# Kernel optimization log

Measured on AMD Instinct MI355X. Metric: run time of the kernel, lower is better.

The kernel has to match this reference:

```python
import math
import jax, jax.numpy as jnp
import numpy as np

B, T, N_FEAT, H = 16, 1024, 512, 8
D_K = N_FEAT // H  # 64


def setup_inputs() -> dict:
    key = jax.random.key(0)
    ks = jax.random.split(key, 16)
    s = 0.02
    return {
        "query": jax.random.normal(ks[0], (B, T, N_FEAT), jnp.float32),
        "key": jax.random.normal(ks[1], (B, T, N_FEAT), jnp.float32),
        "value": jax.random.normal(ks[2], (B, T, N_FEAT), jnp.float32),
        "pos_emb": jax.random.normal(ks[3], (1, T, N_FEAT), jnp.float32),
        "mask": jnp.zeros((B, 1, T), jnp.float32),  # additive bias, 0 = attend
        "Wq": jax.random.normal(ks[4], (N_FEAT, N_FEAT), jnp.float32) * s,
        "bq": jnp.zeros((N_FEAT,), jnp.float32),
        "Wk": jax.random.normal(ks[5], (N_FEAT, N_FEAT), jnp.float32) * s,
        "bk": jnp.zeros((N_FEAT,), jnp.float32),
        "Wv": jax.random.normal(ks[6], (N_FEAT, N_FEAT), jnp.float32) * s,
        "bv": jnp.zeros((N_FEAT,), jnp.float32),
        "Wo": jax.random.normal(ks[7], (N_FEAT, N_FEAT), jnp.float32) * s,
        "bo": jnp.zeros((N_FEAT,), jnp.float32),
        "Wpos": jax.random.normal(ks[8], (N_FEAT, N_FEAT), jnp.float32) * s,
        "pos_bias_u": jax.random.normal(ks[9], (H, D_K), jnp.float32) * 0.05,
        "pos_bias_v": jax.random.normal(ks[10], (H, D_K), jnp.float32) * 0.05,
    }


def reference(query, key, value, pos_emb, mask,
              Wq, bq, Wk, bk, Wv, bv, Wo, bo, Wpos,
              pos_bias_u, pos_bias_v):
    b, t, _ = query.shape
    h, d_k = pos_bias_u.shape
    # projections -> head-split
    q = (query @ Wq + bq).reshape(b, t, h, d_k)                 # (B,T,H,D)
    k = (key @ Wk + bk).reshape(b, -1, h, d_k).transpose(0, 2, 1, 3)    # (B,H,S,D)
    v = (value @ Wv + bv).reshape(b, -1, h, d_k).transpose(0, 2, 1, 3)  # (B,H,S,D)
    p = (pos_emb @ Wpos).reshape(pos_emb.shape[1], h, d_k).transpose(1, 0, 2)  # (H,S,D)
    # Transformer-XL content/position biased queries
    q_u = (q + pos_bias_u).transpose(0, 2, 1, 3)  # (B,H,T,D)
    q_v = (q + pos_bias_v).transpose(0, 2, 1, 3)  # (B,H,T,D)
    matrix_ac = jnp.einsum('bhtd,bhsd->bhts', q_u, k)
    matrix_bd = jnp.einsum('bhtd,hsd->bhts', q_v, p)
    scores = (matrix_ac + matrix_bd) / math.sqrt(d_k) + mask[:, None]  # (B,H,T,S)
    attn = jax.nn.softmax(scores, axis=-1)
    out = jnp.einsum('bhts,bhsd->bthd', attn, v).reshape(b, t, h * d_k)
    return out @ Wo + bo  # (B,T,n_feat)
```

## Files before the change

kernel.cpp:

```cpp
#include <hip/hip_runtime.h>

#define BB 16
#define TT 1024
#define HH 8
#define DD 64
#define NF 512

typedef __attribute__((ext_vector_type(4))) float f4;
typedef __attribute__((ext_vector_type(8))) short s8;
typedef __attribute__((ext_vector_type(2))) unsigned int u32x2;
typedef unsigned short u16;
typedef unsigned int u32;

#define LOG2E 1.4426950408889634f

__device__ __forceinline__ u16 f2bf(float x){
    unsigned int u = __builtin_bit_cast(unsigned int, x);
    u = (u + 0x7FFFu + ((u >> 16) & 1u)) >> 16;
    return (u16)u;
}
__device__ __forceinline__ float bf2f(u16 h){
    unsigned int u = ((unsigned int)h) << 16;
    return __builtin_bit_cast(float, u);
}
__device__ __forceinline__ u32 cvt_pk(float a, float b){
    u32 r; asm("v_cvt_pk_bf16_f32 %0, %1, %2" : "=v"(r) : "v"(a), "v"(b)); return r;
}
__device__ __forceinline__ float lo_bf(u32 p){ return __builtin_bit_cast(float, p << 16); }
__device__ __forceinline__ float hi_bf(u32 p){ return __builtin_bit_cast(float, p & 0xFFFF0000u); }

__global__ __launch_bounds__(256) void prep_w(const float* __restrict__ Wq,
    const float* __restrict__ Wk, const float* __restrict__ Wv,
    const float* __restrict__ Wpos, const float* __restrict__ Wo,
    u16* __restrict__ wtq, u16* __restrict__ wtk, u16* __restrict__ wtv,
    u16* __restrict__ wtp, u16* __restrict__ wohi, u16* __restrict__ wolo)
{
    __shared__ float tile[32][33];
    const int which = blockIdx.z;
    const float* W = which==0?Wq:which==1?Wk:which==2?Wv:which==3?Wpos:Wo;
    const int n0 = blockIdx.x*32, k0 = blockIdx.y*32;
    const int tc = threadIdx.x & 31, tr = threadIdx.x >> 5;
#pragma unroll
    for (int i=0;i<4;i++){ int r = tr + i*8; tile[r][tc] = W[(size_t)(k0+r)*NF + n0+tc]; }
    __syncthreads();
#pragma unroll
    for (int i=0;i<4;i++){
        int n = tr + i*8, k = tc;
        float val = tile[k][n];
        u16 hi = f2bf(val);
        size_t off = (size_t)(n0+n)*NF + k0+k;
        if (which==0) wtq[off]=hi; else if (which==1) wtk[off]=hi;
        else if (which==2) wtv[off]=hi; else if (which==3) wtp[off]=hi;
        else { wohi[off]=hi; wolo[off]=f2bf(val - bf2f(hi)); }
    }
}

template<int MODE>
__global__ __launch_bounds__(256) void gemm_bf16(const float* __restrict__ A,
                                                 const u16* __restrict__ Wt,
                                                 const float* __restrict__ bias,
                                                 const u16* __restrict__ padd,
                                                 u16* __restrict__ out)
{
    __shared__ __align__(16) u16 As[128*64];
    __shared__ __align__(16) u16 Bs[128*64];
    const int tid = threadIdx.x;
    const int row0 = blockIdx.x*128, col0 = blockIdx.y*128;
    const int wid = tid>>6, lane = tid&63, lm = lane&15, lg = lane>>4;
    const int wm = wid>>1, wn = wid&1;

    f4 acc[4][4];
#pragma unroll
    for (int i=0;i<4;i++)
#pragma unroll
        for (int j=0;j<4;j++) acc[i][j] = (f4){0.f,0.f,0.f,0.f};

    for (int k0=0;k0<NF;k0+=64){
        f4 areg[8]; s8 breg[4];
#pragma unroll
        for (int it=0; it<8; ++it){
            int idx = (it*256 + tid)*4;
            int m = idx>>6, k = idx&63;
            areg[it] = *(const f4*)(&A[(size_t)(row0+m)*NF + k0 + k]);
        }
#pragma unroll
        for (int it=0; it<4; ++it){
            int idx = (it*256 + tid)*8;
            int n = idx>>6, k = idx&63;
            breg[it] = *(const s8*)(&Wt[(size_t)(col0+n)*NF + k0 + k]);
        }
        __syncthreads();
#pragma unroll
        for (int it=0; it<8; ++it){
            int idx = (it*256+tid)*4;
            int m = idx>>6, k = idx&63;
            u32x2 pk;
            pk[0] = cvt_pk(areg[it][0], areg[it][1]);
            pk[1] = cvt_pk(areg[it][2], areg[it][3]);
            *(u32x2*)((char*)As + ((m*128 + k*2) ^ ((m&7)<<4))) = pk;
        }
#pragma unroll
        for (int it=0; it<4; ++it){
            int idx = (it*256+tid)*8;
            int n = idx>>6, k = idx&63;
            *(s8*)((char*)Bs + ((n*128 + k*2) ^ ((n&7)<<4))) = breg[it];
        }
        __syncthreads();
        s8 af[4][2], bf[4][2];
#pragma unroll
        for (int i=0;i<4;i++){
            int m = wm*64 + i*16 + lm;
#pragma unroll
            for (int c=0;c<2;c++)
                af[i][c] = *(const s8*)((char*)As + ((m*128 + c*64 + lg*16) ^ ((m&7)<<4)));
        }
#pragma unroll
        for (int j=0;j<4;j++){
            int n = wn*64 + j*16 + lm;
#pragma unroll
            for (int c=0;c<2;c++)
                bf[j][c] = *(const s8*)((char*)Bs + ((n*128 + c*64 + lg*16) ^ ((n&7)<<4)));
        }
#pragma unroll
        for (int i=0;i<4;i++)
#pragma unroll
            for (int j=0;j<4;j++)
#pragma unroll
                for (int c=0;c<2;c++)
                    acc[i][j] = __builtin_amdgcn_mfma_f32_16x16x32_bf16(af[i][c], bf[j][c], acc[i][j], 0,0,0);
    }

#pragma unroll
    for (int i=0;i<4;i++){
#pragma unroll
        for (int j=0;j<4;j++){
#pragma unroll
            for (int r=0;r<4;r++){
                const int m = row0 + wm*64 + i*16 + lg*4 + r;
                const int n = col0 + wn*64 + j*16 + lm;
                float val = acc[i][j][r];
                const int hh = n>>6, dd = n&63;
                if (MODE == 0){
                    out[(size_t)(hh*TT + m)*64 + dd] = f2bf(val);
                } else {
                    val += bias[n];
                    const int b_ = m>>10, t_ = m&1023;
                    if (MODE == 2) val += bf2f(padd[(size_t)(hh*TT + t_)*64 + dd]);
                    if (MODE == 3)
                        out[(((size_t)(b_*HH+hh))*DD + dd)*TT + t_] = f2bf(val);
                    else
                        out[((size_t)(b_*HH+hh)*TT + t_)*64 + dd] = f2bf(val);
                }
            }
        }
    }
}

__global__ __launch_bounds__(256) void gemm_final(const float* __restrict__ A,
    const u16* __restrict__ Bhg, const u16* __restrict__ Blg,
    const float* __restrict__ bias, float* __restrict__ out)
{
    __shared__ __align__(16) u16 Ah[128*64];
    __shared__ __align__(16) u16 Al[128*64];
    __shared__ __align__(16) u16 Bh[128*64];
    __shared__ __align__(16) u16 Bl[128*64];
    const int tid = threadIdx.x;
    const int row0 = blockIdx.x*128, col0 = blockIdx.y*128;
    const int wid = tid>>6, lane = tid&63, lm = lane&15, lg = lane>>4;
    const int wm = wid>>1, wn = wid&1;

    f4 acc[4][4];
#pragma unroll
    for (int i=0;i<4;i++)
#pragma unroll
        for (int j=0;j<4;j++) acc[i][j] = (f4){0.f,0.f,0.f,0.f};

    for (int k0=0;k0<NF;k0+=64){
        f4 areg[8]; s8 bhreg[4], blreg[4];
#pragma unroll
        for (int it=0; it<8; ++it){
            int idx = (it*256 + tid)*4;
            int m = idx>>6, k = idx&63;
            areg[it] = *(const f4*)(&A[(size_t)(row0+m)*NF + k0 + k]);
        }
#pragma unroll
        for (int it=0; it<4; ++it){
            int idx = (it*256 + tid)*8;
            int n = idx>>6, k = idx&63;
            bhreg[it] = *(const s8*)(&Bhg[(size_t)(col0+n)*NF + k0 + k]);
            blreg[it] = *(const s8*)(&Blg[(size_t)(col0+n)*NF + k0 + k]);
        }
        __syncthreads();
#pragma unroll
        for (int it=0; it<8; ++it){
            int idx = (it*256+tid)*4;
            int m = idx>>6, k = idx&63;
            u32 p0 = cvt_pk(areg[it][0], areg[it][1]);
            u32 p1 = cvt_pk(areg[it][2], areg[it][3]);
            u32 q0 = cvt_pk(areg[it][0]-lo_bf(p0), areg[it][1]-hi_bf(p0));
            u32 q1 = cvt_pk(areg[it][2]-lo_bf(p1), areg[it][3]-hi_bf(p1));
            int off = (m*128 + k*2) ^ ((m&7)<<4);
            *(u32x2*)((char*)Ah + off) = (u32x2){p0,p1};
            *(u32x2*)((char*)Al + off) = (u32x2){q0,q1};
        }
#pragma unroll
        for (int it=0; it<4; ++it){
            int idx = (it*256+tid)*8;
            int n = idx>>6, k = idx&63;
            int off = (n*128 + k*2) ^ ((n&7)<<4);
            *(s8*)((char*)Bh + off) = bhreg[it];
            *(s8*)((char*)Bl + off) = blreg[it];
        }
        __syncthreads();
#pragma unroll
        for (int c=0;c<2;c++){
            s8 ah[4], al[4], bh4[4], bl4[4];
#pragma unroll
            for (int i=0;i<4;i++){
                int m = wm*64 + i*16 + lm;
                int off = (m*128 + c*64 + lg*16) ^ ((m&7)<<4);
                ah[i] = *(const s8*)((char*)Ah + off);
                al[i] = *(const s8*)((char*)Al + off);
            }
#pragma unroll
            for (int j=0;j<4;j++){
                int n = wn*64 + j*16 + lm;
                int off = (n*128 + c*64 + lg*16) ^ ((n&7)<<4);
                bh4[j] = *(const s8*)((char*)Bh + off);
                bl4[j] = *(const s8*)((char*)Bl + off);
            }
#pragma unroll
            for (int i=0;i<4;i++)
#pragma unroll
                for (int j=0;j<4;j++){
                    acc[i][j] = __builtin_amdgcn_mfma_f32_16x16x32_bf16(al[i], bh4[j], acc[i][j], 0,0,0);
                    acc[i][j] = __builtin_amdgcn_mfma_f32_16x16x32_bf16(ah[i], bl4[j], acc[i][j], 0,0,0);
                    acc[i][j] = __builtin_amdgcn_mfma_f32_16x16x32_bf16(ah[i], bh4[j], acc[i][j], 0,0,0);
                }
        }
    }

#pragma unroll
    for (int i=0;i<4;i++)
#pragma unroll
        for (int j=0;j<4;j++)
#pragma unroll
            for (int r=0;r<4;r++){
                const int m = row0 + wm*64 + i*16 + lg*4 + r;
                const int n = col0 + wn*64 + j*16 + lm;
                out[(size_t)m*NF + n] = acc[i][j][r] + bias[n];
            }
}

__global__ __launch_bounds__(256) void sbias_kernel(const u16* __restrict__ kp,
                                                    const u16* __restrict__ p,
                                                    const float* __restrict__ pbu,
                                                    const float* __restrict__ pbv,
                                                    const float* __restrict__ mask,
                                                    float* __restrict__ sb)
{
    const int w    = blockIdx.x * 4 + (threadIdx.x >> 6);
    const int lane = threadIdx.x & 63;
    const int s = w & 1023;
    const int h = (w >> 10) & 7;
    const int b = w >> 13;
    const float u  = pbu[h * 64 + lane];
    const float wv = pbv[h * 64 + lane] - u;
    const float kv = bf2f(kp[((size_t)(b * HH + h) * TT + s) * 64 + lane]);
    const float pv = bf2f(p[(size_t)(h * TT + s) * 64 + lane]);
    float val = u * kv + wv * pv;
#pragma unroll
    for (int off = 32; off; off >>= 1) val += __shfl_xor(val, off);
    if (lane == 0)
        sb[(size_t)(b * HH + h) * TT + s] = (val * 0.125f + mask[b * TT + s]) * LOG2E;
}

#define ATTN_GLOAD(tile) do { \
  _Pragma("unroll") for (int it=0; it<2; ++it){ \
    int idx = (it*256+tid)*8; int row_ = idx>>6, col_ = idx&63; \
    kh[it] = *(const s8*)(kb + (size_t)((tile)*64+row_)*64 + col_); \
    vh[it] = *(const s8*)(vtb + (size_t)row_*TT + (tile)*64 + col_); } } while(0)

#define ATTN_SSTORE(buf) do { \
  _Pragma("unroll") for (int it=0; it<2; ++it){ \
    int idx = (it*256+tid)*8; int row_ = idx>>6, col_ = idx&63; \
    int off_ = (row_*128 + col_*2) ^ ((row_&7)<<4); \
    *(s8*)((char*)Ks[(buf)] + off_) = kh[it]; \
    *(s8*)((char*)Vt[(buf)] + off_) = vh[it]; } } while(0)

#define ATTN_QK(buf, scv) do { \
  _Pragma("unroll") for (int j=0;j<4;j++){ \
    int srow_ = j*16+lm; \
    s8 kf0 = *(const s8*)((char*)Ks[(buf)] + ((srow_*128 + lg*16) ^ ((srow_&7)<<4))); \
    s8 kf1 = *(const s8*)((char*)Ks[(buf)] + ((srow_*128 + 64 + lg*16) ^ ((srow_&7)<<4))); \
    scv[j] = __builtin_amdgcn_mfma_f32_16x16x32_bf16(kf0, qf[0], scv[j], 0,0,0); \
    scv[j] = __builtin_amdgcn_mfma_f32_16x16x32_bf16(kf1, qf[1], scv[j], 0,0,0); } } while(0)

__global__ __launch_bounds__(256,3) void attn4(const u16* __restrict__ q,
                                               const u16* __restrict__ kp,
                                               const u16* __restrict__ vt,
                                               const float* __restrict__ sb,
                                               float* __restrict__ ao)
{
    __shared__ __align__(16) u16 Ks[2][64*64];
    __shared__ __align__(16) u16 Vt[2][64*64];
    __shared__ __align__(16) u16 Ps[64*64];

    const int tid = threadIdx.x;
    const int wid = tid>>6, lane = tid&63, lm = lane&15, lg = lane>>4;
    const int bid = blockIdx.x;
    const int xcd = bid & 7, slot = bid >> 3;
    const int bh = xcd + 8*(slot >> 4);
    const int qt = slot & 15;
    const int t0 = qt*64;
    const int b = bh >> 3, h = bh & 7;
    const u16* qb  = q  + (size_t)bh*TT*64;
    const u16* kb  = kp + (size_t)bh*TT*64;
    const u16* vtb = vt + (size_t)bh*DD*TT;
    const float* sbb = sb + (size_t)bh*TT;

    s8 qf[2];
    qf[0] = *(const s8*)(qb + (size_t)(t0 + wid*16 + lm)*64 + lg*8);
    qf[1] = *(const s8*)(qb + (size_t)(t0 + wid*16 + lm)*64 + 32 + lg*8);

    float m_r = -1e30f, l_r = 0.f;
    f4 oacc[4];
#pragma unroll
    for (int n=0;n<4;n++) oacc[n] = (f4){0.f,0.f,0.f,0.f};
    f4 sc_cur[4], sc_next[4];

    const float SCL = 0.125f * LOG2E;
    const int prow = wid*16 + lm;

    s8 kh[2], vh[2];

    ATTN_GLOAD(0);
    ATTN_SSTORE(0);
    ATTN_GLOAD(1);
    __syncthreads();
#pragma unroll
    for (int j=0;j<4;j++) sc_cur[j] = (f4){0.f,0.f,0.f,0.f};
    ATTN_QK(0, sc_cur);

    for (int i=0; i<16; ++i){
        const int cur = i & 1, nxt = cur ^ 1;

        if (i < 15) ATTN_SSTORE(nxt);
        if (i < 14) ATTN_GLOAD(i+2);
        __syncthreads();

        f4 sbf[4];
#pragma unroll
        for (int j=0;j<4;j++) sbf[j] = *(const f4*)(sbb + i*64 + 16*j + 4*lg);

        if (i < 15){
#pragma unroll
            for (int j=0;j<4;j++) sc_next[j] = (f4){0.f,0.f,0.f,0.f};
            __builtin_amdgcn_s_setprio(1);
            ATTN_QK(nxt, sc_next);
            __builtin_amdgcn_s_setprio(0);
        }

        s8 vtf[4][2];
#pragma unroll
        for (int n=0;n<4;n++){
            int drow = n*16 + lm;
#pragma unroll
            for (int c=0;c<2;c++)
                vtf[n][c] = *(const s8*)((char*)Vt[cur] + ((drow*128 + c*64 + lg*16) ^ ((drow&7)<<4)));
        }

        f4 x[4];
#pragma unroll
        for (int j=0;j<4;j++)
#pragma unroll
            for (int r=0;r<4;r++) x[j][r] = sc_cur[j][r]*SCL + sbf[j][r];
        float rm = -1e30f;
#pragma unroll
        for (int r=0;r<4;r++)
            rm = fmaxf(rm, fmaxf(fmaxf(x[0][r], x[1][r]), fmaxf(x[2][r], x[3][r])));
        rm = fmaxf(rm, __shfl_xor(rm, 16));
        rm = fmaxf(rm, __shfl_xor(rm, 32));
        const float nm = fmaxf(m_r, rm);
        const float cf = __builtin_exp2f(m_r - nm);
        m_r = nm;
        f4 p[4];
#pragma unroll
        for (int j=0;j<4;j++)
#pragma unroll
            for (int r=0;r<4;r++) p[j][r] = __builtin_exp2f(x[j][r] - nm);
        f4 sv = p[0] + p[1] + p[2] + p[3];
        float rs = (sv[0]+sv[1]) + (sv[2]+sv[3]);
        rs += __shfl_xor(rs, 16);
        rs += __shfl_xor(rs, 32);
        l_r = l_r*cf + rs;
#pragma unroll
        for (int n=0;n<4;n++) oacc[n] *= cf;

#pragma unroll
        for (int j=0;j<4;j++){
            u32x2 w;
            w[0] = cvt_pk(p[j][0], p[j][1]);
            w[1] = cvt_pk(p[j][2], p[j][3]);
            *(u32x2*)((char*)Ps + ((prow*128 + (16*j + 4*lg)*2) ^ ((prow&7)<<4))) = w;
        }
        s8 pf0 = *(const s8*)((char*)Ps + ((prow*128 +  0 + lg*16) ^ ((prow&7)<<4)));
        s8 pf1 = *(const s8*)((char*)Ps + ((prow*128 + 64 + lg*16) ^ ((prow&7)<<4)));

        __builtin_amdgcn_s_setprio(1);
#pragma unroll
        for (int n=0;n<4;n++){
            oacc[n] = __builtin_amdgcn_mfma_f32_16x16x32_bf16(vtf[n][0], pf0, oacc[n], 0,0,0);
            oacc[n] = __builtin_amdgcn_mfma_f32_16x16x32_bf16(vtf[n][1], pf1, oacc[n], 0,0,0);
        }
        __builtin_amdgcn_s_setprio(0);

        __syncthreads();
#pragma unroll
        for (int j=0;j<4;j++) sc_cur[j] = sc_next[j];
    }

    const float inv = 1.f / l_r;
    const size_t row = (size_t)(b*TT + t0 + wid*16 + lm)*NF + h*64;
#pragma unroll
    for (int n=0; n<4; ++n){
        f4 o = oacc[n] * inv;
        *(f4*)(&ao[row + n*16 + lg*4]) = o;
    }
}

extern "C" void kernel_launch(void* const* d_in, const int* in_sizes, int n_in,
                              void* d_out, int out_size, void* d_ws, size_t ws_size,
                              hipStream_t stream)
{
    const float* query   = (const float*)d_in[0];
    const float* key     = (const float*)d_in[1];
    const float* value   = (const float*)d_in[2];
    const float* pos_emb = (const float*)d_in[3];
    const float* mask    = (const float*)d_in[4];
    const float* Wq   = (const float*)d_in[5];
    const float* bq   = (const float*)d_in[6];
    const float* Wk   = (const float*)d_in[7];
    const float* bk   = (const float*)d_in[8];
    const float* Wv   = (const float*)d_in[9];
    const float* bv   = (const float*)d_in[10];
    const float* Wo   = (const float*)d_in[11];
    const float* bo   = (const float*)d_in[12];
    const float* Wpos = (const float*)d_in[13];
    const float* pbu  = (const float*)d_in[14];
    const float* pbv  = (const float*)d_in[15];
    float* out = (float*)d_out;

    char* ws = (char*)d_ws;
    size_t o = 0;
    u16* wtq  = (u16*)(ws + o); o += (size_t)NF*NF*2;
    u16* wtk  = (u16*)(ws + o); o += (size_t)NF*NF*2;
    u16* wtv  = (u16*)(ws + o); o += (size_t)NF*NF*2;
    u16* wtp  = (u16*)(ws + o); o += (size_t)NF*NF*2;
    u16* wohi = (u16*)(ws + o); o += (size_t)NF*NF*2;
    u16* wolo = (u16*)(ws + o); o += (size_t)NF*NF*2;
    u16* p_ws  = (u16*)(ws + o); o += (size_t)HH*TT*DD*2;
    u16* q_ws  = (u16*)(ws + o); o += (size_t)BB*HH*TT*DD*2;
    u16* kp_ws = (u16*)(ws + o); o += (size_t)BB*HH*TT*DD*2;
    u16* vt_ws = (u16*)(ws + o); o += (size_t)BB*HH*TT*DD*2;
    float* sb_ws = (float*)(ws + o); o += (size_t)BB*HH*TT*4;
    float* ao_ws = (float*)(ws + o); o += (size_t)BB*TT*NF*4;

    const dim3 blk(256);

    prep_w<<<dim3(16,16,5), blk, 0, stream>>>(Wq, Wk, Wv, Wpos, Wo,
                                              wtq, wtk, wtv, wtp, wohi, wolo);
    gemm_bf16<0><<<dim3(TT/128, 4), blk, 0, stream>>>(pos_emb, wtp, nullptr, nullptr, p_ws);
    gemm_bf16<1><<<dim3(BB*TT/128, 4), blk, 0, stream>>>(query, wtq, bq, nullptr, q_ws);
    gemm_bf16<2><<<dim3(BB*TT/128, 4), blk, 0, stream>>>(key,   wtk, bk, p_ws,    kp_ws);
    gemm_bf16<3><<<dim3(BB*TT/128, 4), blk, 0, stream>>>(value, wtv, bv, nullptr, vt_ws);
    sbias_kernel<<<dim3(BB*HH*TT/4), blk, 0, stream>>>(kp_ws, p_ws, pbu, pbv, mask, sb_ws);
    attn4<<<dim3(BB*HH*TT/64), blk, 0, stream>>>(q_ws, kp_ws, vt_ws, sb_ws, ao_ws);
    gemm_final<<<dim3(BB*TT/128, 4), blk, 0, stream>>>(ao_ws, wohi, wolo, bo, out);
}
```

Before: 204.0 us.

## Process 128 query rows per attention block and drop online-softmax max tracking

The attention kernel now gives each wave two 16-row query groups, so a block covers 128 queries. Each K/V tile staged in shared memory is therefore reused across twice as many rows, and the grid is halved. The running-max rescaling of online softmax is removed: probabilities are exp2 of the raw scaled scores and are normalised by a sum taken once at the end. The software-pipelined QK of the next tile is also dropped in favour of computing QK on the current tile. Skipping max subtraction can overflow for large scores and gives 0/0 for fully masked rows, and there is less overlap between the QK and PV stages.

```diff
diff --git a/kernel.cpp b/kernel.cpp
--- a/kernel.cpp
+++ b/kernel.cpp
@@ -288,15 +288,7 @@
     *(s8*)((char*)Ks[(buf)] + off_) = kh[it]; \
     *(s8*)((char*)Vt[(buf)] + off_) = vh[it]; } } while(0)
 
-#define ATTN_QK(buf, scv) do { \
-  _Pragma("unroll") for (int j=0;j<4;j++){ \
-    int srow_ = j*16+lm; \
-    s8 kf0 = *(const s8*)((char*)Ks[(buf)] + ((srow_*128 + lg*16) ^ ((srow_&7)<<4))); \
-    s8 kf1 = *(const s8*)((char*)Ks[(buf)] + ((srow_*128 + 64 + lg*16) ^ ((srow_&7)<<4))); \
-    scv[j] = __builtin_amdgcn_mfma_f32_16x16x32_bf16(kf0, qf[0], scv[j], 0,0,0); \
-    scv[j] = __builtin_amdgcn_mfma_f32_16x16x32_bf16(kf1, qf[1], scv[j], 0,0,0); } } while(0)
-
-__global__ __launch_bounds__(256,3) void attn4(const u16* __restrict__ q,
+__global__ __launch_bounds__(256,3) void attn5(const u16* __restrict__ q,
                                                const u16* __restrict__ kp,
                                                const u16* __restrict__ vt,
                                                const float* __restrict__ sb,
@@ -304,33 +296,38 @@
 {
     __shared__ __align__(16) u16 Ks[2][64*64];
     __shared__ __align__(16) u16 Vt[2][64*64];
-    __shared__ __align__(16) u16 Ps[64*64];
+    __shared__ __align__(16) u16 Ps[128*64];
 
     const int tid = threadIdx.x;
     const int wid = tid>>6, lane = tid&63, lm = lane&15, lg = lane>>4;
     const int bid = blockIdx.x;
     const int xcd = bid & 7, slot = bid >> 3;
-    const int bh = xcd + 8*(slot >> 4);
-    const int qt = slot & 15;
-    const int t0 = qt*64;
+    const int bh = xcd + 8*(slot >> 3);
+    const int qt = slot & 7;
+    const int t0 = qt*128;
     const int b = bh >> 3, h = bh & 7;
     const u16* qb  = q  + (size_t)bh*TT*64;
     const u16* kb  = kp + (size_t)bh*TT*64;
     const u16* vtb = vt + (size_t)bh*DD*TT;
     const float* sbb = sb + (size_t)bh*TT;
 
-    s8 qf[2];
-    qf[0] = *(const s8*)(qb + (size_t)(t0 + wid*16 + lm)*64 + lg*8);
-    qf[1] = *(const s8*)(qb + (size_t)(t0 + wid*16 + lm)*64 + 32 + lg*8);
-
-    float m_r = -1e30f, l_r = 0.f;
-    f4 oacc[4];
-#pragma unroll
-    for (int n=0;n<4;n++) oacc[n] = (f4){0.f,0.f,0.f,0.f};
-    f4 sc_cur[4], sc_next[4];
+    s8 qf[2][2];
+#pragma unroll
+    for (int g=0; g<2; ++g)
+#pragma unroll
+        for (int c=0; c<2; ++c)
+            qf[g][c] = *(const s8*)(qb + (size_t)(t0 + wid*32 + g*16 + lm)*64 + 32*c + lg*8);
+
+    f4 lsum4[2];
+    lsum4[0] = (f4){0.f,0.f,0.f,0.f};
+    lsum4[1] = (f4){0.f,0.f,0.f,0.f};
+    f4 oacc[2][4];
+#pragma unroll
+    for (int g=0;g<2;g++)
+#pragma unroll
+        for (int n=0;n<4;n++) oacc[g][n] = (f4){0.f,0.f,0.f,0.f};
 
     const float SCL = 0.125f * LOG2E;
-    const int prow = wid*16 + lm;
 
     s8 kh[2], vh[2];
 
@@ -338,9 +335,6 @@
     ATTN_SSTORE(0);
     ATTN_GLOAD(1);
     __syncthreads();
-#pragma unroll
-    for (int j=0;j<4;j++) sc_cur[j] = (f4){0.f,0.f,0.f,0.f};
-    ATTN_QK(0, sc_cur);
 
     for (int i=0; i<16; ++i){
         const int cur = i & 1, nxt = cur ^ 1;
@@ -353,13 +347,23 @@
 #pragma unroll
         for (int j=0;j<4;j++) sbf[j] = *(const f4*)(sbb + i*64 + 16*j + 4*lg);
 
-        if (i < 15){
-#pragma unroll
-            for (int j=0;j<4;j++) sc_next[j] = (f4){0.f,0.f,0.f,0.f};
-            __builtin_amdgcn_s_setprio(1);
-            ATTN_QK(nxt, sc_next);
-            __builtin_amdgcn_s_setprio(0);
-        }
+        f4 sc[2][4];
+#pragma unroll
+        for (int g=0;g<2;g++)
+#pragma unroll
+            for (int j=0;j<4;j++) sc[g][j] = (f4){0.f,0.f,0.f,0.f};
+        __builtin_amdgcn_s_setprio(1);
+#pragma unroll
+        for (int j=0;j<4;j++){
+            int srow = j*16+lm;
+            s8 kf0 = *(const s8*)((char*)Ks[cur] + ((srow*128 +      lg*16) ^ ((srow&7)<<4)));
+            s8 kf1 = *(const s8*)((char*)Ks[cur] + ((srow*128 + 64 + lg*16) ^ ((srow&7)<<4)));
+            sc[0][j] = __builtin_amdgcn_mfma_f32_16x16x32_bf16(kf0, qf[0][0], sc[0][j], 0,0,0);
+            sc[0][j] = __builtin_amdgcn_mfma_f32_16x16x32_bf16(kf1, qf[0][1], sc[0][j], 0,0,0);
+            sc[1][j] = __builtin_amdgcn_mfma_f32_16x16x32_bf16(kf0, qf[1][0], sc[1][j], 0,0,0);
+            sc[1][j] = __builtin_amdgcn_mfma_f32_16x16x32_bf16(kf1, qf[1][1], sc[1][j], 0,0,0);
+        }
+        __builtin_amdgcn_s_setprio(0);
 
         s8 vtf[4][2];
 #pragma unroll
@@ -370,62 +374,49 @@
                 vtf[n][c] = *(const s8*)((char*)Vt[cur] + ((drow*128 + c*64 + lg*16) ^ ((drow&7)<<4)));
         }
 
-        f4 x[4];
-#pragma unroll
-        for (int j=0;j<4;j++)
-#pragma unroll
-            for (int r=0;r<4;r++) x[j][r] = sc_cur[j][r]*SCL + sbf[j][r];
-        float rm = -1e30f;
-#pragma unroll
-        for (int r=0;r<4;r++)
-            rm = fmaxf(rm, fmaxf(fmaxf(x[0][r], x[1][r]), fmaxf(x[2][r], x[3][r])));
-        rm = fmaxf(rm, __shfl_xor(rm, 16));
-        rm = fmaxf(rm, __shfl_xor(rm, 32));
-        const float nm = fmaxf(m_r, rm);
-        const float cf = __builtin_exp2f(m_r - nm);
-        m_r = nm;
-        f4 p[4];
-#pragma unroll
-        for (int j=0;j<4;j++)
-#pragma unroll
-            for (int r=0;r<4;r++) p[j][r] = __builtin_exp2f(x[j][r] - nm);
-        f4 sv = p[0] + p[1] + p[2] + p[3];
-        float rs = (sv[0]+sv[1]) + (sv[2]+sv[3]);
-        rs += __shfl_xor(rs, 16);
-        rs += __shfl_xor(rs, 32);
-        l_r = l_r*cf + rs;
-#pragma unroll
-        for (int n=0;n<4;n++) oacc[n] *= cf;
-
-#pragma unroll
-        for (int j=0;j<4;j++){
-            u32x2 w;
-            w[0] = cvt_pk(p[j][0], p[j][1]);
-            w[1] = cvt_pk(p[j][2], p[j][3]);
-            *(u32x2*)((char*)Ps + ((prow*128 + (16*j + 4*lg)*2) ^ ((prow&7)<<4))) = w;
-        }
-        s8 pf0 = *(const s8*)((char*)Ps + ((prow*128 +  0 + lg*16) ^ ((prow&7)<<4)));
-        s8 pf1 = *(const s8*)((char*)Ps + ((prow*128 + 64 + lg*16) ^ ((prow&7)<<4)));
-
-        __builtin_amdgcn_s_setprio(1);
-#pragma unroll
-        for (int n=0;n<4;n++){
-            oacc[n] = __builtin_amdgcn_mfma_f32_16x16x32_bf16(vtf[n][0], pf0, oacc[n], 0,0,0);
-            oacc[n] = __builtin_amdgcn_mfma_f32_16x16x32_bf16(vtf[n][1], pf1, oacc[n], 0,0,0);
-        }
-        __builtin_amdgcn_s_setprio(0);
-
-        __syncthreads();
-#pragma unroll
-        for (int j=0;j<4;j++) sc_cur[j] = sc_next[j];
-    }
-
-    const float inv = 1.f / l_r;
-    const size_t row = (size_t)(b*TT + t0 + wid*16 + lm)*NF + h*64;
-#pragma unroll
-    for (int n=0; n<4; ++n){
-        f4 o = oacc[n] * inv;
-        *(f4*)(&ao[row + n*16 + lg*4]) = o;
+#pragma unroll
+        for (int g=0; g<2; ++g){
+            const int prow = wid*32 + g*16 + lm;
+            f4 p[4];
+#pragma unroll
+            for (int j=0;j<4;j++)
+#pragma unroll
+                for (int r=0;r<4;r++)
+                    p[j][r] = __builtin_exp2f(sc[g][j][r]*SCL + sbf[j][r]);
+            lsum4[g] += (p[0] + p[1]) + (p[2] + p[3]);
+#pragma unroll
+            for (int j=0;j<4;j++){
+                u32x2 w;
+                w[0] = cvt_pk(p[j][0], p[j][1]);
+                w[1] = cvt_pk(p[j][2], p[j][3]);
+                *(u32x2*)((char*)Ps + ((prow*128 + (16*j + 4*lg)*2) ^ ((prow&7)<<4))) = w;
+            }
+            s8 pf0 = *(const s8*)((char*)Ps + ((prow*128 +      lg*16) ^ ((prow&7)<<4)));
+            s8 pf1 = *(const s8*)((char*)Ps + ((prow*128 + 64 + lg*16) ^ ((prow&7)<<4)));
+            __builtin_amdgcn_s_setprio(1);
+#pragma unroll
+            for (int n=0;n<4;n++){
+                oacc[g][n] = __builtin_amdgcn_mfma_f32_16x16x32_bf16(vtf[n][0], pf0, oacc[g][n], 0,0,0);
+                oacc[g][n] = __builtin_amdgcn_mfma_f32_16x16x32_bf16(vtf[n][1], pf1, oacc[g][n], 0,0,0);
+            }
+            __builtin_amdgcn_s_setprio(0);
+        }
+
+        __syncthreads();
+    }
+
+#pragma unroll
+    for (int g=0; g<2; ++g){
+        float ls = (lsum4[g][0]+lsum4[g][1]) + (lsum4[g][2]+lsum4[g][3]);
+        ls += __shfl_xor(ls, 16);
+        ls += __shfl_xor(ls, 32);
+        const float inv = 1.f / ls;
+        const size_t row = (size_t)(b*TT + t0 + wid*32 + g*16 + lm)*NF + h*64;
+#pragma unroll
+        for (int n=0; n<4; ++n){
+            f4 o = oacc[g][n] * inv;
+            *(f4*)(&ao[row + n*16 + lg*4]) = o;
+        }
     }
 }
 
@@ -475,6 +466,6 @@
     gemm_bf16<2><<<dim3(BB*TT/128, 4), blk, 0, stream>>>(key,   wtk, bk, p_ws,    kp_ws);
     gemm_bf16<3><<<dim3(BB*TT/128, 4), blk, 0, stream>>>(value, wtv, bv, nullptr, vt_ws);
     sbias_kernel<<<dim3(BB*HH*TT/4), blk, 0, stream>>>(kp_ws, p_ws, pbu, pbv, mask, sb_ws);
-    attn4<<<dim3(BB*HH*TT/64), blk, 0, stream>>>(q_ws, kp_ws, vt_ws, sb_ws, ao_ws);
+    attn5<<<dim3(BB*HH*TT/128), blk, 0, stream>>>(q_ws, kp_ws, vt_ws, sb_ws, ao_ws);
     gemm_final<<<dim3(BB*TT/128, 4), blk, 0, stream>>>(ao_ws, wohi, wolo, bo, out);
 }
```

Result: slower. 253.8 us (+24.4%).
